# Optimization experiments

Hardware: AMD Instinct MI355X
Metric: run time of the kernel (lower is better)

Reference implementation:

```python
import jax, jax.numpy as jnp
import numpy as np

B, S, D_MODEL = 4, 2048, 128
NUM_HEADS, HEAD_DIM = 4, 32
EPS = 1e-6


def setup_inputs() -> dict:
    key = jax.random.key(0)
    ks = jax.random.split(key, 5)
    scale = 1.0 / np.sqrt(D_MODEL)
    return {
        "x": jax.random.normal(ks[0], (B, S, D_MODEL), dtype=jnp.float32),
        "Wq": jax.random.normal(ks[1], (D_MODEL, NUM_HEADS * HEAD_DIM), dtype=jnp.float32) * scale,
        "bq": jnp.zeros((NUM_HEADS * HEAD_DIM,), dtype=jnp.float32),
        "Wk": jax.random.normal(ks[2], (D_MODEL, NUM_HEADS * HEAD_DIM), dtype=jnp.float32) * scale,
        "bk": jnp.zeros((NUM_HEADS * HEAD_DIM,), dtype=jnp.float32),
        "Wv": jax.random.normal(ks[3], (D_MODEL, NUM_HEADS * HEAD_DIM), dtype=jnp.float32) * scale,
        "bv": jnp.zeros((NUM_HEADS * HEAD_DIM,), dtype=jnp.float32),
        "gamma": jnp.ones((D_MODEL,), dtype=jnp.float32),
        "beta": jnp.zeros((D_MODEL,), dtype=jnp.float32),
        "Wo": jax.random.normal(ks[4], (NUM_HEADS * HEAD_DIM, D_MODEL), dtype=jnp.float32) * scale,
        "bo": jnp.zeros((D_MODEL,), dtype=jnp.float32),
    }


def _split_heads(t):
    # [B, S, H*D] -> [B, H, S, D]
    b, s, _ = t.shape
    return t.reshape(b, s, NUM_HEADS, HEAD_DIM).transpose(0, 2, 1, 3)


def reference(x, Wq, bq, Wk, bk, Wv, bv, gamma, beta, Wo, bo):
    # Pre-LayerNorm (Keras LayerNormalization, eps=1e-6)
    mu = jnp.mean(x, axis=-1, keepdims=True)
    var = jnp.mean(jnp.square(x - mu), axis=-1, keepdims=True)
    xn = (x - mu) * jax.lax.rsqrt(var + EPS) * gamma + beta

    q = _split_heads(xn @ Wq + bq)  # [B,H,S,Dh]
    k = _split_heads(xn @ Wk + bk)
    v = _split_heads(xn @ Wv + bv)

    scores = jnp.einsum("bhqd,bhkd->bhqk", q, k) / jnp.sqrt(jnp.float32(HEAD_DIM))
    attn = jax.nn.softmax(scores, axis=-1)  # [B,H,S,S]
    ctx = jnp.einsum("bhqk,bhkd->bhqd", attn, v)  # [B,H,S,Dh]

    # merge heads -> [B,S,H*Dh]
    ctx = ctx.transpose(0, 2, 1, 3).reshape(x.shape[0], x.shape[1], NUM_HEADS * HEAD_DIM)
    out = ctx @ Wo + bo
    return out + x  # residual
```

## Files before the change

### kernel.cpp

```cpp
#include <hip/hip_runtime.h>

#define D_MODEL 128
#define SEQ 2048
#define NH 4
#define DH 32
#define NBATCH 4
#define BHN 16

typedef __attribute__((ext_vector_type(8))) short bf16x8;
typedef __attribute__((ext_vector_type(4))) float f32x4;
typedef __attribute__((ext_vector_type(4))) unsigned short u16x4;
typedef __attribute__((ext_vector_type(8))) unsigned short u16x8;

#define QSCALE (0.17677669529663687f * 1.4426950408889634f)

static __device__ __forceinline__ unsigned short f2bf_rne(float f) {
    union { float f; unsigned int u; } v; v.f = f;
    unsigned int r = v.u + 0x7FFFu + ((v.u >> 16) & 1u);
    return (unsigned short)(r >> 16);
}


__global__ __launch_bounds__(256) void k0_prep(
    const float* __restrict__ Wq, const float* __restrict__ Wk,
    const float* __restrict__ Wv, const float* __restrict__ Wo,
    unsigned short* __restrict__ wf)
{
    int tid = blockIdx.x * 256 + threadIdx.x;
    int nt = tid >> 8, kk = (tid >> 6) & 3, lane = tid & 63;
    int col = lane & 15, quad = lane >> 4;
    const float* W = (nt < 8) ? Wq : (nt < 16) ? Wk : (nt < 24) ? Wv : Wo;
    int n = (nt & 7) * 16 + col;
    u16x8 v;
    #pragma unroll
    for (int j = 0; j < 8; ++j)
        v[j] = f2bf_rne(W[(kk * 32 + quad * 8 + j) * 128 + n]);
    *(u16x8*)(wf + (size_t)tid * 8) = v;
}

__global__ __launch_bounds__(256) void k1_ln_qkv(
    const float* __restrict__ x, const unsigned short* __restrict__ wf,
    const float* __restrict__ bq, const float* __restrict__ bk,
    const float* __restrict__ bv,
    const float* __restrict__ gamma, const float* __restrict__ beta,
    unsigned short* __restrict__ qf_ws, unsigned short* __restrict__ kf_ws,
    unsigned short* __restrict__ vf_ws)
{
    __shared__ __align__(16) unsigned short xsh[16][136];
    const int t = threadIdx.x, w = t >> 6, lane = t & 63;
    const int row0 = blockIdx.x * 16;
    const float g0 = gamma[lane], g1 = gamma[lane + 64];
    const float be0 = beta[lane], be1 = beta[lane + 64];
    #pragma unroll
    for (int i = 0; i < 4; ++i) {
        int r = w * 4 + i;
        const float* xr = x + (size_t)(row0 + r) * 128;
        float x0 = xr[lane], x1 = xr[lane + 64];
        float s = x0 + x1, s2 = x0 * x0 + x1 * x1;
        #pragma unroll
        for (int off = 32; off > 0; off >>= 1) {
            s += __shfl_xor(s, off);
            s2 += __shfl_xor(s2, off);
        }
        float mu  = s * (1.0f / 128.0f);
        float var = s2 * (1.0f / 128.0f) - mu * mu;
        float rs  = rsqrtf(var + 1e-6f);
        xsh[r][lane]      = f2bf_rne((x0 - mu) * rs * g0 + be0);
        xsh[r][lane + 64] = f2bf_rne((x1 - mu) * rs * g1 + be1);
    }
    __syncthreads();

    const int col = lane & 15, quad = lane >> 4;
    bf16x8 a[4];
    #pragma unroll
    for (int kk = 0; kk < 4; ++kk)
        a[kk] = *(const bf16x8*)&xsh[col][kk * 32 + quad * 8];

    const int row_g0 = row0 + quad * 4;
    const int b = row_g0 >> 11;
    const int s0 = row_g0 & (SEQ - 1);
    const int nt0 = w * 6;

    for (int nt = nt0; nt < nt0 + 6; ++nt) {
        int n = nt * 16 + col;
        const unsigned short* wrow = wf + (size_t)(nt * 4) * 512 + lane * 8;
        f32x4 c = {0.f, 0.f, 0.f, 0.f};
        #pragma unroll
        for (int kk = 0; kk < 4; ++kk) {
            bf16x8 bfr = *(const bf16x8*)(wrow + kk * 512);
            c = __builtin_amdgcn_mfma_f32_16x16x32_bf16(a[kk], bfr, c, 0, 0, 0);
        }
        int m = nt >> 3;
        int nn = n & 127, h = nn >> 5, dh = nn & 31, bh = b * NH + h;
        if (m == 0) {
            float bias = bq[nn];
            #pragma unroll
            for (int r = 0; r < 4; ++r) {
                int s = s0 + r;
                size_t idx = ((size_t)(bh * 128 + (s >> 4)) * 64
                              + (dh >> 3) * 16 + (s & 15)) * 8 + (dh & 7);
                qf_ws[idx] = f2bf_rne((c[r] + bias) * QSCALE);
            }
        } else if (m == 1) {
            float bias = bk[nn];
            #pragma unroll
            for (int r = 0; r < 4; ++r) {
                int s = s0 + r;
                size_t idx = ((size_t)((bh * 64 + (s >> 5)) * 2 + (s & 1)) * 64
                              + (dh >> 3) * 16 + ((s & 31) >> 1)) * 8 + (dh & 7);
                kf_ws[idx] = f2bf_rne(c[r] + bias);
            }
        } else {
            float bias = bv[nn];
            u16x4 pv;
            #pragma unroll
            for (int r = 0; r < 4; ++r) pv[r] = f2bf_rne(c[r] + bias);
            size_t idx = ((size_t)((bh * 64 + (s0 >> 5)) * 2 + (dh >> 4)) * 64
                          + ((s0 & 31) >> 3) * 16 + (dh & 15)) * 8 + (s0 & 7);
            *(u16x4*)(vf_ws + idx) = pv;
        }
    }
}

__global__ __launch_bounds__(256) void k2_attn(
    const unsigned short* __restrict__ qf_ws,
    const unsigned short* __restrict__ kf_ws,
    const unsigned short* __restrict__ vf_ws,
    unsigned short* __restrict__ ctx_f)
{
    __shared__ __align__(16) unsigned int p_sh[4][32][36];
    __shared__ __align__(16) float comb[4][32][33];
    __shared__ float lsh[4][32];
    const int w = threadIdx.x >> 6, lane = threadIdx.x & 63;
    const int col = lane & 15, quad = lane >> 4;
    const int hf = w;
    const int bh = blockIdx.y;
    const int qi = blockIdx.x * 2;

    const unsigned short* qb = qf_ws + (size_t)(bh * 128 + qi) * 512;
    const unsigned short* kb = kf_ws + (size_t)bh * 65536;
    const unsigned short* vb = vf_ws + (size_t)bh * 65536;

    bf16x8 qf0 = *(const bf16x8*)(qb + lane * 8);
    bf16x8 qf1 = *(const bf16x8*)(qb + 512 + lane * 8);

    f32x4 c00 = {0.f,0.f,0.f,0.f}, c01 = {0.f,0.f,0.f,0.f};
    f32x4 c10 = {0.f,0.f,0.f,0.f}, c11 = {0.f,0.f,0.f,0.f};
    float l0[4] = {0.f,0.f,0.f,0.f}, l1[4] = {0.f,0.f,0.f,0.f};

    const int kbi0 = hf * 16;
    bf16x8 kf0 = *(const bf16x8*)(kb + (size_t)kbi0 * 1024 + lane * 8);
    bf16x8 kf1 = *(const bf16x8*)(kb + (size_t)kbi0 * 1024 + 512 + lane * 8);
    bf16x8 vf0 = *(const bf16x8*)(vb + (size_t)kbi0 * 1024 + lane * 8);
    bf16x8 vf1 = *(const bf16x8*)(vb + (size_t)kbi0 * 1024 + 512 + lane * 8);

    for (int it = 0; it < 16; ++it) {
        int nkbi = kbi0 + ((it + 1) & 15);
        bf16x8 nkf0 = *(const bf16x8*)(kb + (size_t)nkbi * 1024 + lane * 8);
        bf16x8 nkf1 = *(const bf16x8*)(kb + (size_t)nkbi * 1024 + 512 + lane * 8);
        bf16x8 nvf0 = *(const bf16x8*)(vb + (size_t)nkbi * 1024 + lane * 8);
        bf16x8 nvf1 = *(const bf16x8*)(vb + (size_t)nkbi * 1024 + 512 + lane * 8);

        f32x4 z = {0.f,0.f,0.f,0.f};
        f32x4 s00 = __builtin_amdgcn_mfma_f32_16x16x32_bf16(qf0, kf0, z, 0, 0, 0);
        f32x4 s01 = __builtin_amdgcn_mfma_f32_16x16x32_bf16(qf0, kf1, z, 0, 0, 0);
        f32x4 s10 = __builtin_amdgcn_mfma_f32_16x16x32_bf16(qf1, kf0, z, 0, 0, 0);
        f32x4 s11 = __builtin_amdgcn_mfma_f32_16x16x32_bf16(qf1, kf1, z, 0, 0, 0);
        #pragma unroll
        for (int r = 0; r < 4; ++r) {
            float p00 = __builtin_amdgcn_exp2f(s00[r]);
            float p01 = __builtin_amdgcn_exp2f(s01[r]);
            l0[r] += p00 + p01;
            p_sh[w][quad * 4 + r][col] =
                (__float_as_uint(p00) >> 16) | (__float_as_uint(p01) & 0xFFFF0000u);
            float p10 = __builtin_amdgcn_exp2f(s10[r]);
            float p11 = __builtin_amdgcn_exp2f(s11[r]);
            l1[r] += p10 + p11;
            p_sh[w][16 + quad * 4 + r][col] =
                (__float_as_uint(p10) >> 16) | (__float_as_uint(p11) & 0xFFFF0000u);
        }
        bf16x8 pf0 = *(const bf16x8*)&p_sh[w][col][quad * 4];
        bf16x8 pf1 = *(const bf16x8*)&p_sh[w][16 + col][quad * 4];
        c00 = __builtin_amdgcn_mfma_f32_16x16x32_bf16(pf0, vf0, c00, 0, 0, 0);
        c01 = __builtin_amdgcn_mfma_f32_16x16x32_bf16(pf0, vf1, c01, 0, 0, 0);
        c10 = __builtin_amdgcn_mfma_f32_16x16x32_bf16(pf1, vf0, c10, 0, 0, 0);
        c11 = __builtin_amdgcn_mfma_f32_16x16x32_bf16(pf1, vf1, c11, 0, 0, 0);
        kf0 = nkf0; kf1 = nkf1; vf0 = nvf0; vf1 = nvf1;
    }

    #pragma unroll
    for (int r = 0; r < 4; ++r) {
        #pragma unroll
        for (int off = 1; off < 16; off <<= 1) {
            l0[r] += __shfl_xor(l0[r], off);
            l1[r] += __shfl_xor(l1[r], off);
        }
    }
    #pragma unroll
    for (int r = 0; r < 4; ++r) {
        int rr = quad * 4 + r;
        comb[hf][rr][col]           = c00[r];
        comb[hf][rr][16 + col]      = c01[r];
        comb[hf][16 + rr][col]      = c10[r];
        comb[hf][16 + rr][16 + col] = c11[r];
    }
    if (col == 0) {
        #pragma unroll
        for (int r = 0; r < 4; ++r) {
            lsh[hf][quad * 4 + r]      = l0[r];
            lsh[hf][16 + quad * 4 + r] = l1[r];
        }
    }
    __syncthreads();
    {
        int row = threadIdx.x >> 3;
        int cg = threadIdx.x & 7;
        int d0 = cg * 4;
        float linv = 1.0f / (lsh[0][row] + lsh[1][row] + lsh[2][row] + lsh[3][row]);
        u16x4 ov;
        #pragma unroll
        for (int j = 0; j < 4; ++j) {
            int cc = d0 + j;
            ov[j] = f2bf_rne((comb[0][row][cc] + comb[1][row][cc]
                            + comb[2][row][cc] + comb[3][row][cc]) * linv);
        }
        int s_loc = blockIdx.x * 32 + row;
        int b = bh >> 2, h = bh & 3;
        int s_g = b * SEQ + s_loc;
        size_t idx = (((size_t)(s_g >> 4) * 4 + h) * 64
                      + (d0 >> 3) * 16 + (s_g & 15)) * 8 + (d0 & 7);
        *(u16x4*)(ctx_f + idx) = ov;
    }
}

__global__ __launch_bounds__(256) void k3_out(
    const unsigned short* __restrict__ ctx_f,
    const unsigned short* __restrict__ wf, const float* __restrict__ bo,
    const float* __restrict__ x, float* __restrict__ out)
{
    const int t = threadIdx.x, w = t >> 6, lane = t & 63;
    const int col = lane & 15, quad = lane >> 4;
    const int mt = blockIdx.x;
    bf16x8 a[4];
    #pragma unroll
    for (int kk = 0; kk < 4; ++kk)
        a[kk] = *(const bf16x8*)(ctx_f + ((size_t)(mt * 4 + kk) * 64 + lane) * 8);
    #pragma unroll
    for (int i = 0; i < 2; ++i) {
        int ntl = w * 2 + i;
        int nt_g = 24 + ntl;
        int n = ntl * 16 + col;
        f32x4 c = {0.f, 0.f, 0.f, 0.f};
        #pragma unroll
        for (int kk = 0; kk < 4; ++kk) {
            bf16x8 bfr = *(const bf16x8*)(wf + ((size_t)(nt_g * 4 + kk) * 64 + lane) * 8);
            c = __builtin_amdgcn_mfma_f32_16x16x32_bf16(a[kk], bfr, c, 0, 0, 0);
        }
        float bias = bo[n];
        #pragma unroll
        for (int r = 0; r < 4; ++r) {
            size_t row_g = (size_t)mt * 16 + quad * 4 + r;
            out[row_g * 128 + n] = c[r] + bias + x[row_g * 128 + n];
        }
    }
}

extern "C" void kernel_launch(void* const* d_in, const int* in_sizes, int n_in,
                              void* d_out, int out_size, void* d_ws, size_t ws_size,
                              hipStream_t stream) {
    const float* x     = (const float*)d_in[0];
    const float* Wq    = (const float*)d_in[1];
    const float* bq    = (const float*)d_in[2];
    const float* Wk    = (const float*)d_in[3];
    const float* bk    = (const float*)d_in[4];
    const float* Wv    = (const float*)d_in[5];
    const float* bv    = (const float*)d_in[6];
    const float* gamma = (const float*)d_in[7];
    const float* beta  = (const float*)d_in[8];
    const float* Wo    = (const float*)d_in[9];
    const float* bo    = (const float*)d_in[10];
    float* out = (float*)d_out;

    const size_t QKV_ELEMS = (size_t)BHN * SEQ * DH;
    unsigned short* qf_ws = (unsigned short*)d_ws;
    unsigned short* kf_ws = qf_ws + QKV_ELEMS;
    unsigned short* vf_ws = kf_ws + QKV_ELEMS;
    unsigned short* ctx_f = vf_ws + QKV_ELEMS;
    unsigned short* wf    = ctx_f + QKV_ELEMS;

    k0_prep<<<32, 256, 0, stream>>>(Wq, Wk, Wv, Wo, wf);
    k1_ln_qkv<<<512, 256, 0, stream>>>(x, wf, bq, bk, bv, gamma, beta,
                                       qf_ws, kf_ws, vf_ws);
    k2_attn<<<dim3(SEQ / 32, BHN), 256, 0, stream>>>(qf_ws, kf_ws, vf_ws, ctx_f);
    k3_out<<<512, 256, 0, stream>>>(ctx_f, wf, bo, x, out);
}
```

Measured before the change: 108.7 us.

## Fuse attention and output projection into one kernel covering all heads per block

Merges the attention kernel and the output-projection kernel. Each 512-thread block now handles one batch, a 32-query tile and all four heads, with two waves per head, each taking half the keys. The context is normalized into shared memory and fed straight into the Wo MFMA, so the ctx round trip through global memory and one launch go away. The cost is a 4x smaller grid (256 blocks), a longer serial key loop per wave (32 iterations instead of 16) and more shared memory per block, which can lower occupancy.

```diff
diff --git a/kernel.cpp b/kernel.cpp
--- a/kernel.cpp
+++ b/kernel.cpp
@@ -122,24 +122,30 @@
     }
 }
 
-__global__ __launch_bounds__(256) void k2_attn(
+__global__ __launch_bounds__(512) void k23_attn_out(
     const unsigned short* __restrict__ qf_ws,
     const unsigned short* __restrict__ kf_ws,
     const unsigned short* __restrict__ vf_ws,
-    unsigned short* __restrict__ ctx_f)
+    const unsigned short* __restrict__ wf,
+    const float* __restrict__ bo, const float* __restrict__ x,
+    float* __restrict__ out)
 {
-    __shared__ __align__(16) unsigned int p_sh[4][32][36];
-    __shared__ __align__(16) float comb[4][32][33];
-    __shared__ float lsh[4][32];
+    __shared__ __align__(16) unsigned int p_sh[8][32][36];
+    __shared__ __align__(16) float comb[8][32][33];
+    __shared__ float lsh[8][32];
+    __shared__ __align__(16) unsigned short ctx_sh[32][136];
+
     const int w = threadIdx.x >> 6, lane = threadIdx.x & 63;
     const int col = lane & 15, quad = lane >> 4;
-    const int hf = w;
-    const int bh = blockIdx.y;
+    const int h = w >> 1, kh = w & 1;
+    const int b = blockIdx.y;
+    const int bh = b * NH + h;
+    const int q0 = blockIdx.x * 32;
     const int qi = blockIdx.x * 2;
 
     const unsigned short* qb = qf_ws + (size_t)(bh * 128 + qi) * 512;
-    const unsigned short* kb = kf_ws + (size_t)bh * 65536;
-    const unsigned short* vb = vf_ws + (size_t)bh * 65536;
+    const unsigned short* kb0 = kf_ws + (size_t)bh * 65536 + (size_t)(kh * 32) * 1024;
+    const unsigned short* vb0 = vf_ws + (size_t)bh * 65536 + (size_t)(kh * 32) * 1024;
 
     bf16x8 qf0 = *(const bf16x8*)(qb + lane * 8);
     bf16x8 qf1 = *(const bf16x8*)(qb + 512 + lane * 8);
@@ -148,18 +154,20 @@
     f32x4 c10 = {0.f,0.f,0.f,0.f}, c11 = {0.f,0.f,0.f,0.f};
     float l0[4] = {0.f,0.f,0.f,0.f}, l1[4] = {0.f,0.f,0.f,0.f};
 
-    const int kbi0 = hf * 16;
-    bf16x8 kf0 = *(const bf16x8*)(kb + (size_t)kbi0 * 1024 + lane * 8);
-    bf16x8 kf1 = *(const bf16x8*)(kb + (size_t)kbi0 * 1024 + 512 + lane * 8);
-    bf16x8 vf0 = *(const bf16x8*)(vb + (size_t)kbi0 * 1024 + lane * 8);
-    bf16x8 vf1 = *(const bf16x8*)(vb + (size_t)kbi0 * 1024 + 512 + lane * 8);
-
-    for (int it = 0; it < 16; ++it) {
-        int nkbi = kbi0 + ((it + 1) & 15);
-        bf16x8 nkf0 = *(const bf16x8*)(kb + (size_t)nkbi * 1024 + lane * 8);
-        bf16x8 nkf1 = *(const bf16x8*)(kb + (size_t)nkbi * 1024 + 512 + lane * 8);
-        bf16x8 nvf0 = *(const bf16x8*)(vb + (size_t)nkbi * 1024 + lane * 8);
-        bf16x8 nvf1 = *(const bf16x8*)(vb + (size_t)nkbi * 1024 + 512 + lane * 8);
+    const unsigned short* pk = kb0;
+    const unsigned short* pv = vb0;
+    bf16x8 kf0 = *(const bf16x8*)(pk + lane * 8);
+    bf16x8 kf1 = *(const bf16x8*)(pk + 512 + lane * 8);
+    bf16x8 vf0 = *(const bf16x8*)(pv + lane * 8);
+    bf16x8 vf1 = *(const bf16x8*)(pv + 512 + lane * 8);
+
+    for (int it = 0; it < 32; ++it) {
+        const unsigned short* nk = (it == 31) ? kb0 : pk + 1024;
+        const unsigned short* nv = (it == 31) ? vb0 : pv + 1024;
+        bf16x8 nkf0 = *(const bf16x8*)(nk + lane * 8);
+        bf16x8 nkf1 = *(const bf16x8*)(nk + 512 + lane * 8);
+        bf16x8 nvf0 = *(const bf16x8*)(nv + lane * 8);
+        bf16x8 nvf1 = *(const bf16x8*)(nv + 512 + lane * 8);
 
         f32x4 z = {0.f,0.f,0.f,0.f};
         f32x4 s00 = __builtin_amdgcn_mfma_f32_16x16x32_bf16(qf0, kf0, z, 0, 0, 0);
@@ -186,6 +194,7 @@
         c10 = __builtin_amdgcn_mfma_f32_16x16x32_bf16(pf1, vf0, c10, 0, 0, 0);
         c11 = __builtin_amdgcn_mfma_f32_16x16x32_bf16(pf1, vf1, c11, 0, 0, 0);
         kf0 = nkf0; kf1 = nkf1; vf0 = nvf0; vf1 = nvf1;
+        pk = nk; pv = nv;
     }
 
     #pragma unroll
@@ -199,57 +208,43 @@
     #pragma unroll
     for (int r = 0; r < 4; ++r) {
         int rr = quad * 4 + r;
-        comb[hf][rr][col]           = c00[r];
-        comb[hf][rr][16 + col]      = c01[r];
-        comb[hf][16 + rr][col]      = c10[r];
-        comb[hf][16 + rr][16 + col] = c11[r];
+        comb[w][rr][col]           = c00[r];
+        comb[w][rr][16 + col]      = c01[r];
+        comb[w][16 + rr][col]      = c10[r];
+        comb[w][16 + rr][16 + col] = c11[r];
     }
     if (col == 0) {
         #pragma unroll
         for (int r = 0; r < 4; ++r) {
-            lsh[hf][quad * 4 + r]      = l0[r];
-            lsh[hf][16 + quad * 4 + r] = l1[r];
+            lsh[w][quad * 4 + r]      = l0[r];
+            lsh[w][16 + quad * 4 + r] = l1[r];
         }
     }
     __syncthreads();
+
     {
-        int row = threadIdx.x >> 3;
-        int cg = threadIdx.x & 7;
-        int d0 = cg * 4;
-        float linv = 1.0f / (lsh[0][row] + lsh[1][row] + lsh[2][row] + lsh[3][row]);
-        u16x4 ov;
-        #pragma unroll
-        for (int j = 0; j < 4; ++j) {
-            int cc = d0 + j;
-            ov[j] = f2bf_rne((comb[0][row][cc] + comb[1][row][cc]
-                            + comb[2][row][cc] + comb[3][row][cc]) * linv);
-        }
-        int s_loc = blockIdx.x * 32 + row;
-        int b = bh >> 2, h = bh & 3;
-        int s_g = b * SEQ + s_loc;
-        size_t idx = (((size_t)(s_g >> 4) * 4 + h) * 64
-                      + (d0 >> 3) * 16 + (s_g & 15)) * 8 + (d0 & 7);
-        *(u16x4*)(ctx_f + idx) = ov;
-    }
-}
-
-__global__ __launch_bounds__(256) void k3_out(
-    const unsigned short* __restrict__ ctx_f,
-    const unsigned short* __restrict__ wf, const float* __restrict__ bo,
-    const float* __restrict__ x, float* __restrict__ out)
-{
-    const int t = threadIdx.x, w = t >> 6, lane = t & 63;
-    const int col = lane & 15, quad = lane >> 4;
-    const int mt = blockIdx.x;
-    bf16x8 a[4];
-    #pragma unroll
-    for (int kk = 0; kk < 4; ++kk)
-        a[kk] = *(const bf16x8*)(ctx_f + ((size_t)(mt * 4 + kk) * 64 + lane) * 8);
-    #pragma unroll
-    for (int i = 0; i < 2; ++i) {
-        int ntl = w * 2 + i;
-        int nt_g = 24 + ntl;
-        int n = ntl * 16 + col;
+        int row = threadIdx.x >> 4;
+        int dg  = (threadIdx.x & 15) * 8;
+        int hh  = dg >> 5;
+        float linv = 1.0f / (lsh[2 * hh][row] + lsh[2 * hh + 1][row]);
+        int dl = dg & 31;
+        u16x8 ov;
+        #pragma unroll
+        for (int j = 0; j < 8; ++j)
+            ov[j] = f2bf_rne((comb[2 * hh][row][dl + j]
+                            + comb[2 * hh + 1][row][dl + j]) * linv);
+        *(u16x8*)&ctx_sh[row][dg] = ov;
+    }
+    __syncthreads();
+
+    #pragma unroll
+    for (int mt = 0; mt < 2; ++mt) {
+        bf16x8 a[4];
+        #pragma unroll
+        for (int kk = 0; kk < 4; ++kk)
+            a[kk] = *(const bf16x8*)&ctx_sh[mt * 16 + col][kk * 32 + quad * 8];
+        int n = w * 16 + col;
+        int nt_g = 24 + w;
         f32x4 c = {0.f, 0.f, 0.f, 0.f};
         #pragma unroll
         for (int kk = 0; kk < 4; ++kk) {
@@ -259,7 +254,7 @@
         float bias = bo[n];
         #pragma unroll
         for (int r = 0; r < 4; ++r) {
-            size_t row_g = (size_t)mt * 16 + quad * 4 + r;
+            size_t row_g = (size_t)b * SEQ + q0 + mt * 16 + quad * 4 + r;
             out[row_g * 128 + n] = c[r] + bias + x[row_g * 128 + n];
         }
     }
@@ -285,12 +280,11 @@
     unsigned short* qf_ws = (unsigned short*)d_ws;
     unsigned short* kf_ws = qf_ws + QKV_ELEMS;
     unsigned short* vf_ws = kf_ws + QKV_ELEMS;
-    unsigned short* ctx_f = vf_ws + QKV_ELEMS;
-    unsigned short* wf    = ctx_f + QKV_ELEMS;
+    unsigned short* wf    = vf_ws + QKV_ELEMS;
 
     k0_prep<<<32, 256, 0, stream>>>(Wq, Wk, Wv, Wo, wf);
     k1_ln_qkv<<<512, 256, 0, stream>>>(x, wf, bq, bk, bv, gamma, beta,
                                        qf_ws, kf_ws, vf_ws);
-    k2_attn<<<dim3(SEQ / 32, BHN), 256, 0, stream>>>(qf_ws, kf_ws, vf_ws, ctx_f);
-    k3_out<<<512, 256, 0, stream>>>(ctx_f, wf, bo, x, out);
-}
+    k23_attn_out<<<dim3(64, 4), 512, 0, stream>>>(qf_ws, kf_ws, vf_ws, wf,
+                                                  bo, x, out);
+}
```

New measurement: 103.6 us. 4.7% less time.
